# Optimization experiments

Hardware: AMD Instinct MI355X
Metric: run time of the kernel (lower is better)

Reference implementation:

```python
import jax, jax.numpy as jnp
import numpy as np

FACTOR = 0.1   # init_kwargs factor
EPS = 1e-7
B, C, H, W = 256, 3, 224, 224


def setup_inputs() -> dict:
    key = jax.random.key(0)
    k1, k2, k3 = jax.random.split(key, 3)
    x = jax.random.normal(k1, (B, C, H, W), dtype=jnp.float32)
    shift_fy = jax.random.uniform(k2, (B,), dtype=jnp.float32)  # maps to torch.rand(1)
    shift_fx = jax.random.uniform(k3, (B,), dtype=jnp.float32)
    return {"x": x, "shift_fy": shift_fy, "shift_fx": shift_fx}


def _shift_axis(img, shift, axis, size):
    # Equivalent to torch in-place slice copy + zero-fill:
    #   shift>0: img[..., :size-shift] = img[..., shift:]; img[..., size-shift:] = 0
    #   shift<0: img[..., -shift:]   = img[..., :shift];  img[..., :-shift]   = 0
    # == roll by -shift, then zero positions j where j+shift is out of [0, size)
    idx = jnp.arange(size)
    rolled = jnp.roll(img, -shift, axis=axis)
    mask = (idx + shift >= 0) & (idx + shift < size)
    shp = [1, 1, 1]
    shp[axis] = size
    return rolled * mask.reshape(shp).astype(img.dtype)


def _per_image(img, fy, fx):
    # img: [C, H, W]
    h, w = img.shape[1], img.shape[2]
    # int(shift_factor * size) truncates toward zero -> jnp.trunc
    sy = jnp.trunc((fy * 2.0 - 1.0) * FACTOR * h).astype(jnp.int32)
    sx = jnp.trunc((fx * 2.0 - 1.0) * FACTOR * w).astype(jnp.int32)
    img = _shift_axis(img, sy, 1, h)
    img = _shift_axis(img, sx, 2, w)
    # standardize with unbiased std (torch.std default, ddof=1)
    n = img.size
    mean = jnp.mean(img)
    var = jnp.sum(jnp.square(img - mean)) / (n - 1)
    img = (img - mean) / (jnp.sqrt(var) + EPS)
    # min-max normalize
    mn = jnp.min(img)
    mx = jnp.max(img)
    return (img - mn) / (mx - mn)


def reference(x, shift_fy, shift_fx):
    # fully vectorized over the batch (original uses a Python per-image loop)
    return jax.vmap(_per_image)(x, shift_fy, shift_fx)
```

## Files before the change

kernel.cpp:

```cpp
#include <hip/hip_runtime.h>
#include <math.h>


constexpr int kC = 3, kH = 224, kW = 224;
constexpr int kCHW = kC * kH * kW;
constexpr int kROWS = kC * kH;
constexpr int kQPR  = kW / 4;
constexpr int kNQ   = kROWS * kQPR;
constexpr int BLOCK = 1024;

template <int R>
__device__ __forceinline__ void phase2(const float* __restrict__ xb,
                                       float* __restrict__ ob,
                                       int sy, int sx, float mn, float inv,
                                       int tid)
{
    for (int f = tid; f < kNQ; f += BLOCK) {
        const int rr = f / kQPR;
        const int q  = f - rr * kQPR;
        const int j  = rr % kH;
        const int c0 = rr - j;
        const int jj = j + sy;
        const bool rowok = (unsigned)jj < (unsigned)kH;
        const int jc = rowok ? jj : 0;
        const float* __restrict__ src = xb + (c0 + jc) * kW;

        const int i0 = q * 4;
        const int base = i0 + sx - R;
        int qa = base;       qa = qa < 0 ? 0 : qa; qa = qa > kW - 4 ? kW - 4 : qa;
        int qb = base + 4;   qb = qb < 0 ? 0 : qb; qb = qb > kW - 4 ? kW - 4 : qb;
        const float4 av = *(const float4*)(src + qa);
        const float4 bv = *(const float4*)(src + qb);
        const float* a = (const float*)&av;
        const float* b = (const float*)&bv;

        float sel[4];
        #pragma unroll
        for (int k = 0; k < 4; ++k)
            sel[k] = (k + R < 4) ? a[k + R] : b[k + R - 4];

        float4 o;
        float* po = (float*)&o;
        #pragma unroll
        for (int k = 0; k < 4; ++k) {
            const int s = i0 + k + sx;
            const float v = (rowok && (unsigned)s < (unsigned)kW) ? sel[k] : 0.0f;
            po[k] = (v - mn) * inv;
        }
        *(float4*)(ob + rr * kW + i0) = o;
    }
}

__global__ __launch_bounds__(BLOCK) void shift_norm(
    const float* __restrict__ x, const float* __restrict__ sfy,
    const float* __restrict__ sfx, float* __restrict__ out)
{
    const int img = blockIdx.x;
    const float* __restrict__ xb = x + (size_t)img * kCHW;
    float* __restrict__ ob = out + (size_t)img * kCHW;

    float ty = sfy[img] * 2.0f - 1.0f; ty *= 0.1f; ty *= (float)kH;
    const int sy = (int)truncf(ty);
    float tx = sfx[img] * 2.0f - 1.0f; tx *= 0.1f; tx *= (float)kW;
    const int sx = (int)truncf(tx);

    const int tid = threadIdx.x;

    const int rlo = sy > 0 ? sy : 0;
    const int rhi = kH + (sy < 0 ? sy : 0);
    const int clo = sx > 0 ? sx : 0;
    const int chi = kW + (sx < 0 ? sx : 0);

    float vmin = INFINITY, vmax = -INFINITY;

    for (int f = tid; f < kNQ; f += BLOCK) {
        const int rr = f / kQPR;
        const int q  = f - rr * kQPR;
        const int j  = rr % kH;
        const bool rok = (j >= rlo) & (j < rhi);
        const float4 v4 = *(const float4*)(xb + rr * kW + q * 4);
        const float* v = (const float*)&v4;
        #pragma unroll
        for (int k = 0; k < 4; ++k) {
            const int i = q * 4 + k;
            const float val = (rok & (i >= clo) & (i < chi)) ? v[k] : 0.0f;
            vmin = fminf(vmin, val);
            vmax = fmaxf(vmax, val);
        }
    }

    #pragma unroll
    for (int off = 32; off > 0; off >>= 1) {
        vmin = fminf(vmin, __shfl_down(vmin, off));
        vmax = fmaxf(vmax, __shfl_down(vmax, off));
    }
    __shared__ float smin[BLOCK / 64], smax[BLOCK / 64];
    __shared__ float s_mn, s_inv;
    const int wave = tid >> 6, lane = tid & 63;
    if (lane == 0) { smin[wave] = vmin; smax[wave] = vmax; }
    __syncthreads();
    if (tid == 0) {
        float mn = smin[0], mx = smax[0];
        #pragma unroll
        for (int w2 = 1; w2 < BLOCK / 64; ++w2) {
            mn = fminf(mn, smin[w2]);
            mx = fmaxf(mx, smax[w2]);
        }
        s_mn = mn;
        s_inv = 1.0f / (mx - mn);
    }
    __syncthreads();
    const float mn = s_mn, inv = s_inv;

    switch (sx & 3) {
        case 0: phase2<0>(xb, ob, sy, sx, mn, inv, tid); break;
        case 1: phase2<1>(xb, ob, sy, sx, mn, inv, tid); break;
        case 2: phase2<2>(xb, ob, sy, sx, mn, inv, tid); break;
        default: phase2<3>(xb, ob, sy, sx, mn, inv, tid); break;
    }
}

extern "C" void kernel_launch(void* const* d_in, const int* in_sizes, int n_in,
                              void* d_out, int out_size, void* d_ws, size_t ws_size,
                              hipStream_t stream) {
    const float* x  = (const float*)d_in[0];
    const float* fy = (const float*)d_in[1];
    const float* fx = (const float*)d_in[2];
    float* out = (float*)d_out;
    const int B = in_sizes[1];
    shift_norm<<<B, BLOCK, 0, stream>>>(x, fy, fx, out);
}
```

Baseline: 296.6 us.

## Split per-image kernel into two-kernel partial min/max and normalize passes

Replaces the single kernel that used one 1024-thread block per image with two kernels, each using 8 blocks of 256 threads per image. The first computes partial min/max values into workspace, and the second combines them and writes the shifted, normalized output. This spreads work over more blocks than the 256 images and removes the in-block barrier between phases. In exchange it adds a second launch and a second full read of the input from global memory, which the first pass may have left in cache.

```diff
diff --git a/kernel.cpp b/kernel.cpp
--- a/kernel.cpp
+++ b/kernel.cpp
@@ -7,15 +7,79 @@
 constexpr int kROWS = kC * kH;
 constexpr int kQPR  = kW / 4;
 constexpr int kNQ   = kROWS * kQPR;
-constexpr int BLOCK = 1024;
+constexpr int TB    = 256;
+constexpr int PARTS = 8;
+
+__device__ __forceinline__ void shifts_for(const float* __restrict__ sfy,
+                                           const float* __restrict__ sfx,
+                                           int img, int& sy, int& sx)
+{
+    float ty = sfy[img] * 2.0f - 1.0f; ty *= 0.1f; ty *= (float)kH;
+    sy = (int)truncf(ty);
+    float tx = sfx[img] * 2.0f - 1.0f; tx *= 0.1f; tx *= (float)kW;
+    sx = (int)truncf(tx);
+}
+
+__global__ __launch_bounds__(TB) void minmax_k(
+    const float* __restrict__ x, const float* __restrict__ sfy,
+    const float* __restrict__ sfx, float2* __restrict__ ws)
+{
+    const int img  = blockIdx.x / PARTS;
+    const int part = blockIdx.x - img * PARTS;
+    const float* __restrict__ xb = x + (size_t)img * kCHW;
+
+    int sy, sx; shifts_for(sfy, sfx, img, sy, sx);
+
+    const int rlo = sy > 0 ? sy : 0;
+    const int rhi = kH + (sy < 0 ? sy : 0);
+    const int clo = sx > 0 ? sx : 0;
+    const int chi = kW + (sx < 0 ? sx : 0);
+
+    float vmin = INFINITY, vmax = -INFINITY;
+
+    for (int f = part * TB + threadIdx.x; f < kNQ; f += PARTS * TB) {
+        const int rr = f / kQPR;
+        const int q  = f - rr * kQPR;
+        const int j  = rr % kH;
+        const bool rok = (j >= rlo) & (j < rhi);
+        const float4 v4 = *(const float4*)(xb + rr * kW + q * 4);
+        const float* v = (const float*)&v4;
+        #pragma unroll
+        for (int k = 0; k < 4; ++k) {
+            const int i = q * 4 + k;
+            const float val = (rok & (i >= clo) & (i < chi)) ? v[k] : 0.0f;
+            vmin = fminf(vmin, val);
+            vmax = fmaxf(vmax, val);
+        }
+    }
+
+    #pragma unroll
+    for (int off = 32; off > 0; off >>= 1) {
+        vmin = fminf(vmin, __shfl_down(vmin, off));
+        vmax = fmaxf(vmax, __shfl_down(vmax, off));
+    }
+    __shared__ float smin[TB / 64], smax[TB / 64];
+    const int wave = threadIdx.x >> 6, lane = threadIdx.x & 63;
+    if (lane == 0) { smin[wave] = vmin; smax[wave] = vmax; }
+    __syncthreads();
+    if (threadIdx.x == 0) {
+        float mn = smin[0], mx = smax[0];
+        #pragma unroll
+        for (int w2 = 1; w2 < TB / 64; ++w2) {
+            mn = fminf(mn, smin[w2]);
+            mx = fmaxf(mx, smax[w2]);
+        }
+        ws[img * PARTS + part] = make_float2(mn, mx);
+    }
+}
 
 template <int R>
-__device__ __forceinline__ void phase2(const float* __restrict__ xb,
-                                       float* __restrict__ ob,
-                                       int sy, int sx, float mn, float inv,
-                                       int tid)
+__device__ __forceinline__ void gather_norm(const float* __restrict__ xb,
+                                            float* __restrict__ ob,
+                                            int sy, int sx, float mn, float inv,
+                                            int f0)
 {
-    for (int f = tid; f < kNQ; f += BLOCK) {
+    for (int f = f0; f < kNQ; f += PARTS * TB) {
         const int rr = f / kQPR;
         const int q  = f - rr * kQPR;
         const int j  = rr % kH;
@@ -51,72 +115,33 @@
     }
 }
 
-__global__ __launch_bounds__(BLOCK) void shift_norm(
+__global__ __launch_bounds__(TB) void norm_k(
     const float* __restrict__ x, const float* __restrict__ sfy,
-    const float* __restrict__ sfx, float* __restrict__ out)
+    const float* __restrict__ sfx, const float2* __restrict__ ws,
+    float* __restrict__ out)
 {
-    const int img = blockIdx.x;
+    const int img  = blockIdx.x / PARTS;
+    const int part = blockIdx.x - img * PARTS;
     const float* __restrict__ xb = x + (size_t)img * kCHW;
     float* __restrict__ ob = out + (size_t)img * kCHW;
 
-    float ty = sfy[img] * 2.0f - 1.0f; ty *= 0.1f; ty *= (float)kH;
-    const int sy = (int)truncf(ty);
-    float tx = sfx[img] * 2.0f - 1.0f; tx *= 0.1f; tx *= (float)kW;
-    const int sx = (int)truncf(tx);
+    int sy, sx; shifts_for(sfy, sfx, img, sy, sx);
 
-    const int tid = threadIdx.x;
+    float mn = INFINITY, mx = -INFINITY;
+    #pragma unroll
+    for (int p = 0; p < PARTS; ++p) {
+        const float2 v = ws[img * PARTS + p];
+        mn = fminf(mn, v.x);
+        mx = fmaxf(mx, v.y);
+    }
+    const float inv = 1.0f / (mx - mn);
 
-    const int rlo = sy > 0 ? sy : 0;
-    const int rhi = kH + (sy < 0 ? sy : 0);
-    const int clo = sx > 0 ? sx : 0;
-    const int chi = kW + (sx < 0 ? sx : 0);
-
-    float vmin = INFINITY, vmax = -INFINITY;
-
-    for (int f = tid; f < kNQ; f += BLOCK) {
-        const int rr = f / kQPR;
-        const int q  = f - rr * kQPR;
-        const int j  = rr % kH;
-        const bool rok = (j >= rlo) & (j < rhi);
-        const float4 v4 = *(const float4*)(xb + rr * kW + q * 4);
-        const float* v = (const float*)&v4;
-        #pragma unroll
-        for (int k = 0; k < 4; ++k) {
-            const int i = q * 4 + k;
-            const float val = (rok & (i >= clo) & (i < chi)) ? v[k] : 0.0f;
-            vmin = fminf(vmin, val);
-            vmax = fmaxf(vmax, val);
-        }
-    }
-
-    #pragma unroll
-    for (int off = 32; off > 0; off >>= 1) {
-        vmin = fminf(vmin, __shfl_down(vmin, off));
-        vmax = fmaxf(vmax, __shfl_down(vmax, off));
-    }
-    __shared__ float smin[BLOCK / 64], smax[BLOCK / 64];
-    __shared__ float s_mn, s_inv;
-    const int wave = tid >> 6, lane = tid & 63;
-    if (lane == 0) { smin[wave] = vmin; smax[wave] = vmax; }
-    __syncthreads();
-    if (tid == 0) {
-        float mn = smin[0], mx = smax[0];
-        #pragma unroll
-        for (int w2 = 1; w2 < BLOCK / 64; ++w2) {
-            mn = fminf(mn, smin[w2]);
-            mx = fmaxf(mx, smax[w2]);
-        }
-        s_mn = mn;
-        s_inv = 1.0f / (mx - mn);
-    }
-    __syncthreads();
-    const float mn = s_mn, inv = s_inv;
-
+    const int f0 = part * TB + threadIdx.x;
     switch (sx & 3) {
-        case 0: phase2<0>(xb, ob, sy, sx, mn, inv, tid); break;
-        case 1: phase2<1>(xb, ob, sy, sx, mn, inv, tid); break;
-        case 2: phase2<2>(xb, ob, sy, sx, mn, inv, tid); break;
-        default: phase2<3>(xb, ob, sy, sx, mn, inv, tid); break;
+        case 0: gather_norm<0>(xb, ob, sy, sx, mn, inv, f0); break;
+        case 1: gather_norm<1>(xb, ob, sy, sx, mn, inv, f0); break;
+        case 2: gather_norm<2>(xb, ob, sy, sx, mn, inv, f0); break;
+        default: gather_norm<3>(xb, ob, sy, sx, mn, inv, f0); break;
     }
 }
 
@@ -128,5 +153,7 @@
     const float* fx = (const float*)d_in[2];
     float* out = (float*)d_out;
     const int B = in_sizes[1];
-    shift_norm<<<B, BLOCK, 0, stream>>>(x, fy, fx, out);
+    float2* ws = (float2*)d_ws;
+    minmax_k<<<B * PARTS, TB, 0, stream>>>(x, fy, fx, ws);
+    norm_k<<<B * PARTS, TB, 0, stream>>>(x, fy, fx, ws, out);
 }
```

Measured after the change: 301.5 us. No clear change (+1.6%).
